# Kernel tuning notes

Hardware: AMD Instinct MI355X
Metric: run time of the kernel (lower is better)

## Reference

```python
import jax, jax.numpy as jnp
import numpy as np

B, T, C, D = 4, 20, 128, 64
TD = T * D  # 1280; adaptor input dim = 2*TD = 2560


def setup_inputs() -> dict:
    key = jax.random.key(0)
    ks = jax.random.split(key, 12)

    def lin(k, out_d, in_d):
        return jax.random.normal(k, (out_d, in_d), jnp.float32) / np.float32(np.sqrt(in_d))

    return {
        "h": jax.random.normal(ks[0], (B, T, C, D), jnp.float32),
        "W1": lin(ks[1], 128, 2 * TD), "b1": jnp.zeros((128,), jnp.float32),
        "W2": lin(ks[2], 256, 128),   "b2": jnp.zeros((256,), jnp.float32),
        "W3": lin(ks[3], 64, 256),    "b3": jnp.zeros((64,), jnp.float32),
        "W4": lin(ks[4], 1, 64),      "b4": jnp.zeros((1,), jnp.float32),
        "A_a": jax.random.normal(ks[5], (C, C), jnp.float32) * 0.01,
        "A_m": jax.random.normal(ks[6], (C, C), jnp.float32) * 0.01,
        "W_add": lin(ks[7], D, D), "b_add": jnp.zeros((D,), jnp.float32),
        "W_mod": lin(ks[8], D, D), "b_mod": jnp.zeros((D,), jnp.float32),
        "beta1": jnp.float32(1.0), "beta2": jnp.float32(1.0), "beta3": jnp.float32(1.0),
    }


def reference(h, W1, b1, W2, b2, W3, b3, W4, b4, A_a, A_m,
              W_add, b_add, W_mod, b_mod, beta1, beta2, beta3):
    Bb, Tt, Cc, Dd = h.shape
    td = Tt * Dd
    # H^(u) flattened over time: (B, C, T*D)
    h_flat = jnp.transpose(h, (0, 2, 1, 3)).reshape(Bb, Cc, td)

    # Adaptor MLP on concat(H^u, H^v). First layer is linear on the concat,
    # so split W1 and broadcast-add instead of materializing (B,C,C,2*T*D).
    W1u, W1v = W1[:, :td], W1[:, td:]
    fu = h_flat @ W1u.T                      # (B, C, 128) contribution of u
    fv = h_flat @ W1v.T                      # (B, C, 128) contribution of v
    x = jax.nn.relu(fu[:, :, None, :] + fv[:, None, :, :] + b1)   # (B, Cu, Cv, 128)
    x = jax.nn.relu(jnp.einsum('buvk,mk->buvm', x, W2) + b2)       # (B, Cu, Cv, 256)
    x = jax.nn.relu(jnp.einsum('buvk,mk->buvm', x, W3) + b3)       # (B, Cu, Cv, 64)
    s = jax.nn.sigmoid(jnp.einsum('buvk,mk->buvm', x, W4) + b4)[..., 0]  # (B, C, C)

    # Add path: a_t^(v) = sum_u S^(u,v) * A_a^(u,v) * h_t^(u)
    w = s * A_a[None]                        # (B, Cu, Cv)
    a = jnp.einsum('buv,btud->btvd', w, h)   # (B, T, C, D)
    a = a @ W_add.T + b_add

    # Modulator path: m_t^(v) = (sum_u A_m^(u,v) h_t^(u)) * h_t^(v)
    m = jnp.einsum('uv,btud->btvd', A_m, h) * h
    m = m @ W_mod.T + b_mod

    return beta1 * h + beta2 * a + beta3 * m
```

## Files before the change

### kernel.cpp

```cpp
#include <hip/hip_runtime.h>
#include <cmath>

#define NB 4
#define NT 20
#define NC 128
#define ND 64
#define TD 1280

typedef short short8 __attribute__((ext_vector_type(8)));
typedef float f32x4 __attribute__((ext_vector_type(4)));

static __device__ __forceinline__ unsigned short f2bf(float f) {
  union { float f; unsigned int u; } v; v.f = f;
  unsigned int r = v.u + 0x7FFFu + ((v.u >> 16) & 1u);
  return (unsigned short)(r >> 16);
}

static __device__ __forceinline__ void conv16(const float* __restrict__ s,
                                              unsigned short* __restrict__ d) {
#pragma unroll
  for (int q = 0; q < 2; q++) {
    float4 f0 = *(const float4*)(s + q * 8);
    float4 f1 = *(const float4*)(s + q * 8 + 4);
    uint4 o;
    o.x = (unsigned)f2bf(f0.x) | ((unsigned)f2bf(f0.y) << 16);
    o.y = (unsigned)f2bf(f0.z) | ((unsigned)f2bf(f0.w) << 16);
    o.z = (unsigned)f2bf(f1.x) | ((unsigned)f2bf(f1.y) << 16);
    o.w = (unsigned)f2bf(f1.z) | ((unsigned)f2bf(f1.w) << 16);
    *(uint4*)(d + q * 8) = o;
  }
}

static __device__ __forceinline__ void conv16_lds(const float* __restrict__ s,
                                                  char* __restrict__ base,
                                                  int byte0, int swz) {
#pragma unroll
  for (int q = 0; q < 2; q++) {
    float4 f0 = *(const float4*)(s + q * 8);
    float4 f1 = *(const float4*)(s + q * 8 + 4);
    uint4 o;
    o.x = (unsigned)f2bf(f0.x) | ((unsigned)f2bf(f0.y) << 16);
    o.y = (unsigned)f2bf(f0.z) | ((unsigned)f2bf(f0.w) << 16);
    o.z = (unsigned)f2bf(f1.x) | ((unsigned)f2bf(f1.y) << 16);
    o.w = (unsigned)f2bf(f1.z) | ((unsigned)f2bf(f1.w) << 16);
    *(uint4*)(base + ((byte0 + q * 16) ^ swz)) = o;
  }
}

__global__ __launch_bounds__(128) void k_front2(
    const float* __restrict__ h, const float* __restrict__ W1,
    const float* __restrict__ W2, const float* __restrict__ W3,
    const float* __restrict__ A_m, const float* __restrict__ W_add,
    const float* __restrict__ W_mod,
    float* __restrict__ fuv,
    unsigned short* __restrict__ W2bf, unsigned short* __restrict__ W3bf,
    unsigned short* __restrict__ A_mTbf, unsigned short* __restrict__ W_addbf,
    unsigned short* __restrict__ W_modbf, unsigned short* __restrict__ hbfT) {
  __shared__ char smem[33280];
  int blk = blockIdx.x, tid = threadIdx.x;
  if (blk < 256) {
    char* atile = smem;
    char* btile = smem + 8192;
    int mtile = blk & 15;
    int ntile = blk >> 4;
    int lane = tid & 63;
    int w = tid >> 6;
    int lr = lane & 15, lhi = lane >> 4;
    int ac = tid >> 2;
    int akseg = (tid & 3) << 5;
    int arow_g = mtile * 32 + ac;
    int ab = arow_g >> 7, acc_c = arow_g & 127;
    int aswz = (ac & 7) << 4;
    int abase = ac * 256 + akseg * 2;
    int bn = tid >> 3;
    int bkseg = (tid & 7) << 4;
    int bn_g = ntile * 16 + bn;
    const float* bsrc_row =
        W1 + (size_t)(bn_g & 127) * (2 * TD) + (bn_g >> 7) * TD;
    int bswz = (bn & 7) << 4;
    int bbase = bn * 256 + bkseg * 2;
    int arow_l = w * 16 + lr;
    int a_rd_base = arow_l * 256;
    int a_rd_swz = (lr & 7) << 4;
    int b_rd_base = lr * 256;

    f32x4 acc = (f32x4){0.f, 0.f, 0.f, 0.f};
    for (int kc = 0; kc < 10; kc++) {
      int k0 = kc * 128;
      if (kc) __syncthreads();
      {
        int t5 = (k0 + akseg) >> 6;
        int d0 = akseg & 63;
        const float* src =
            h + (((size_t)(ab * NT + t5)) * NC + acc_c) * ND + d0;
        conv16_lds(src, atile, abase, aswz);
        conv16_lds(src + 16, atile, abase + 32, aswz);
      }
      conv16_lds(bsrc_row + k0 + bkseg, btile, bbase, bswz);
      __syncthreads();
#pragma unroll
      for (int ks = 0; ks < 4; ks++) {
        int koff = ks * 64 + lhi * 16;
        short8 a = *(const short8*)(atile + a_rd_base + (koff ^ a_rd_swz));
        short8 bv = *(const short8*)(btile + b_rd_base + (koff ^ ((lr & 7) << 4)));
        acc = __builtin_amdgcn_mfma_f32_16x16x32_bf16(a, bv, acc, 0, 0, 0);
      }
    }
    int m0 = mtile * 32 + w * 16 + lhi * 4;
    int n = ntile * 16 + lr;
#pragma unroll
    for (int r = 0; r < 4; r++)
      fuv[(size_t)(m0 + r) * 256 + n] = acc[r];
    return;
  }
  int cb = blk - 256;
  if (cb < 16) {
    size_t i = (size_t)cb * 2048 + tid * 16;
    conv16(W2 + i, W2bf + i);
  } else if (cb < 24) {
    size_t i = (size_t)(cb - 16) * 2048 + tid * 16;
    conv16(W3 + i, W3bf + i);
  } else if (cb < 32) {
    size_t base = (size_t)(cb - 24) * 2048 + tid * 16;
    unsigned short tmp[16];
#pragma unroll
    for (int i2 = 0; i2 < 16; i2++) {
      size_t idx = base + i2;
      int v = (int)(idx >> 7), u = (int)(idx & 127);
      tmp[i2] = f2bf(A_m[(size_t)u * 128 + v]);
    }
    *(uint4*)(A_mTbf + base) = *(uint4*)tmp;
    *(uint4*)(A_mTbf + base + 8) = *(uint4*)(tmp + 8);
  } else if (cb < 34) {
    size_t i = (size_t)(cb - 32) * 2048 + tid * 16;
    conv16(W_add + i, W_addbf + i);
  } else if (cb < 36) {
    size_t i = (size_t)(cb - 34) * 2048 + tid * 16;
    conv16(W_mod + i, W_modbf + i);
  } else {
    float (*hsl)[65] = (float (*)[65])smem;
    int bt = cb - 36;
    const float* hb = h + (size_t)bt * 8192;
    for (int i = tid; i < 8192; i += 128) hsl[i >> 6][i & 63] = hb[i];
    __syncthreads();
    unsigned short* ob = hbfT + (size_t)bt * 8192;
    for (int i = tid; i < 8192; i += 128) {
      int d = i >> 7, u = i & 127;
      ob[i] = f2bf(hsl[u][d]);
    }
  }
}

__global__ __launch_bounds__(512) void k_pair(
    const float* __restrict__ fuv, const float* __restrict__ b1,
    const unsigned short* __restrict__ W2bf, const float* __restrict__ b2,
    const unsigned short* __restrict__ W3bf, const float* __restrict__ b3,
    const float* __restrict__ W4, const float* __restrict__ b4,
    const float* __restrict__ A_a, unsigned short* __restrict__ wTbf) {
  int blk = blockIdx.x;
  int b = blk >> 6;
  int u0 = (blk & 63) << 1;
  __shared__ char ycraw[8][4096];
  __shared__ char w2all[65536];
  __shared__ char w3all[32768];
  int t = threadIdx.x;
  int lane = t & 63;
  int w = t >> 6;
  int uw = u0 + (w >> 2);
  int lr = lane & 15;
  int lhi = lane >> 4;
  int v0w = (w & 3) * 32;
  int sw = (lr & 7) << 4;

  for (int s = w; s < 64; s += 8) {
    int o = s * 1024 + lane * 16;
    int row = o >> 8;
    int cbo = o & 255;
    const char* src = (const char*)W2bf + (size_t)row * 256 +
                      (cbo ^ ((row & 7) << 4));
    __builtin_amdgcn_global_load_lds(src, w2all + s * 1024, 16, 0, 0);
  }
  for (int s = w; s < 32; s += 8) {
    int o = s * 1024 + lane * 16;
    int row = o >> 9;
    int cbo = o & 511;
    const char* src = (const char*)W3bf + (size_t)row * 512 +
                      (cbo ^ ((row & 7) << 4));
    __builtin_amdgcn_global_load_lds(src, w3all + s * 1024, 16, 0, 0);
  }

  short8 xf[4][2];
  {
    const float* fu_base = fuv + ((size_t)(b * NC + uw)) * 256;
#pragma unroll
    for (int ks = 0; ks < 4; ks++) {
      int k0 = ks * 32 + lhi * 8;
      float4 fua = *(const float4*)(fu_base + k0);
      float4 fub4 = *(const float4*)(fu_base + k0 + 4);
      float4 b1a = *(const float4*)(b1 + k0);
      float4 b1b = *(const float4*)(b1 + k0 + 4);
#pragma unroll
      for (int vg = 0; vg < 2; vg++) {
        int v = v0w + vg * 16 + lr;
        const float* fvr = fuv + ((size_t)(b * NC + v)) * 256 + 128 + k0;
        float4 fva = *(const float4*)(fvr);
        float4 fvb = *(const float4*)(fvr + 4);
        float e[8];
        e[0] = fua.x + fva.x + b1a.x; e[1] = fua.y + fva.y + b1a.y;
        e[2] = fua.z + fva.z + b1a.z; e[3] = fua.w + fva.w + b1a.w;
        e[4] = fub4.x + fvb.x + b1b.x; e[5] = fub4.y + fvb.y + b1b.y;
        e[6] = fub4.z + fvb.z + b1b.z; e[7] = fub4.w + fvb.w + b1b.w;
        union { unsigned int pw[4]; short8 s8; } pk;
#pragma unroll
        for (int i2 = 0; i2 < 4; i2++) {
          float lo = e[2 * i2] > 0.f ? e[2 * i2] : 0.f;
          float hi = e[2 * i2 + 1] > 0.f ? e[2 * i2 + 1] : 0.f;
          pk.pw[i2] = (unsigned int)f2bf(lo) | ((unsigned int)f2bf(hi) << 16);
        }
        xf[ks][vg] = pk.s8;
      }
    }
  }
  __syncthreads();

  char* ycb = ycraw[w];
  f32x4 zacc[2][4];
#pragma unroll
  for (int q = 0; q < 2; q++)
#pragma unroll
    for (int n = 0; n < 4; n++) zacc[q][n] = (f32x4){0.f, 0.f, 0.f, 0.f};

  for (int c = 0; c < 4; c++) {
    int mc = c * 64;
    const char* w2base_c = w2all + mc * 256;
    f32x4 yac[4][2];
#pragma unroll
    for (int mt = 0; mt < 4; mt++) {
      yac[mt][0] = (f32x4){0.f, 0.f, 0.f, 0.f};
      yac[mt][1] = (f32x4){0.f, 0.f, 0.f, 0.f};
    }
    __builtin_amdgcn_s_setprio(1);
#pragma unroll
    for (int ks = 0; ks < 4; ks++) {
#pragma unroll
      for (int mt = 0; mt < 4; mt++) {
        int wrow = mt * 16 + lr;
        short8 wv = *(const short8*)(
            w2base_c + wrow * 256 + ((ks * 64 + lhi * 16) ^ ((wrow & 7) << 4)));
        yac[mt][0] = __builtin_amdgcn_mfma_f32_16x16x32_bf16(wv, xf[ks][0], yac[mt][0], 0, 0, 0);
        yac[mt][1] = __builtin_amdgcn_mfma_f32_16x16x32_bf16(wv, xf[ks][1], yac[mt][1], 0, 0, 0);
      }
    }
    __builtin_amdgcn_s_setprio(0);
#pragma unroll
    for (int mt = 0; mt < 4; mt++) {
      float4 b2v = *(const float4*)(b2 + mc + mt * 16 + lhi * 4);
#pragma unroll
      for (int vg = 0; vg < 2; vg++) {
        int v = vg * 16 + lr;
        float e0 = yac[mt][vg][0] + b2v.x; e0 = e0 > 0.f ? e0 : 0.f;
        float e1 = yac[mt][vg][1] + b2v.y; e1 = e1 > 0.f ? e1 : 0.f;
        float e2 = yac[mt][vg][2] + b2v.z; e2 = e2 > 0.f ? e2 : 0.f;
        float e3 = yac[mt][vg][3] + b2v.w; e3 = e3 > 0.f ? e3 : 0.f;
        uint2 pw;
        pw.x = (unsigned)f2bf(e0) | ((unsigned)f2bf(e1) << 16);
        pw.y = (unsigned)f2bf(e2) | ((unsigned)f2bf(e3) << 16);
        int byte = (v * 128 + (mt * 16 + lhi * 4) * 2) ^ ((lr & 7) << 4);
        *(uint2*)(ycb + byte) = pw;
      }
    }
    __builtin_amdgcn_s_setprio(1);
#pragma unroll
    for (int ks2 = 0; ks2 < 2; ks2++) {
      int kb = ks2 * 32 + lhi * 8;
      short8 ya0 = *(const short8*)(ycb + ((lr * 128 + kb * 2) ^ sw));
      short8 ya1 = *(const short8*)(ycb + (((16 + lr) * 128 + kb * 2) ^ sw));
#pragma unroll
      for (int n = 0; n < 4; n++) {
        int jrow = 16 * n + lr;
        short8 w3v = *(const short8*)(
            w3all + jrow * 512 +
            ((mc * 2 + ks2 * 64 + lhi * 16) ^ ((jrow & 7) << 4)));
        zacc[0][n] = __builtin_amdgcn_mfma_f32_16x16x32_bf16(ya0, w3v, zacc[0][n], 0, 0, 0);
        zacc[1][n] = __builtin_amdgcn_mfma_f32_16x16x32_bf16(ya1, w3v, zacc[1][n], 0, 0, 0);
      }
    }
    __builtin_amdgcn_s_setprio(0);
  }

  float sp[2][4];
#pragma unroll
  for (int q = 0; q < 2; q++)
#pragma unroll
    for (int r = 0; r < 4; r++) sp[q][r] = 0.f;
#pragma unroll
  for (int n = 0; n < 4; n++) {
    int j = 16 * n + lr;
    float b3v = b3[j], w4v = W4[j];
#pragma unroll
    for (int q = 0; q < 2; q++)
#pragma unroll
      for (int r = 0; r < 4; r++) {
        float z = zacc[q][n][r] + b3v;
        z = z > 0.f ? z : 0.f;
        sp[q][r] += w4v * z;
      }
  }
#pragma unroll
  for (int mask = 1; mask <= 8; mask <<= 1)
#pragma unroll
    for (int q = 0; q < 2; q++)
#pragma unroll
      for (int r = 0; r < 4; r++)
        sp[q][r] += __shfl_xor(sp[q][r], mask, 64);
  float bb4 = b4[0];
  if (lr == 0) {
#pragma unroll
    for (int q = 0; q < 2; q++)
#pragma unroll
      for (int r = 0; r < 4; r++) {
        int v = v0w + 16 * q + lhi * 4 + r;
        float s = 1.f / (1.f + expf(-(sp[q][r] + bb4)));
        wTbf[((size_t)(b * NC + v)) * NC + uw] = f2bf(s * A_a[uw * NC + v]);
      }
  }
}

__global__ __launch_bounds__(128) void k_out_mfma(
    const float* __restrict__ h, const unsigned short* __restrict__ wTbf,
    const unsigned short* __restrict__ A_mTbf,
    const unsigned short* __restrict__ hbfT,
    const unsigned short* __restrict__ W_addbf,
    const unsigned short* __restrict__ W_modbf,
    const float* __restrict__ b_add, const float* __restrict__ b_mod,
    const float* __restrict__ beta1p, const float* __restrict__ beta2p,
    const float* __restrict__ beta3p, float* __restrict__ out) {
  int blk = blockIdx.x;
  int bt = blk >> 3;
  int v0 = (blk & 7) << 4;
  int b = bt / 20;
  __shared__ char apre_l[2048];
  __shared__ char mpre_l[2048];
  int t = threadIdx.x;
  int lane = t & 63;
  int w = t >> 6;
  int lr = lane & 15, lhi = lane >> 4;
  int nf0 = w * 2;

  f32x4 aacc[2], macc[2];
#pragma unroll
  for (int i = 0; i < 2; i++) {
    aacc[i] = (f32x4){0.f, 0.f, 0.f, 0.f};
    macc[i] = (f32x4){0.f, 0.f, 0.f, 0.f};
  }
  const unsigned short* wrow = wTbf + ((size_t)(b * NC + v0 + lr)) * NC + lhi * 8;
  const unsigned short* arow = A_mTbf + (size_t)(v0 + lr) * NC + lhi * 8;
  const unsigned short* hTrow = hbfT + (size_t)bt * 8192 + lhi * 8;
#pragma unroll
  for (int kb = 0; kb < 128; kb += 32) {
    short8 aw = *(const short8*)(wrow + kb);
    short8 am = *(const short8*)(arow + kb);
#pragma unroll
    for (int nfi = 0; nfi < 2; nfi++) {
      int nf = nf0 + nfi;
      short8 bv = *(const short8*)(hTrow + (size_t)(nf * 16 + lr) * NC + kb);
      aacc[nfi] = __builtin_amdgcn_mfma_f32_16x16x32_bf16(aw, bv, aacc[nfi], 0, 0, 0);
      macc[nfi] = __builtin_amdgcn_mfma_f32_16x16x32_bf16(am, bv, macc[nfi], 0, 0, 0);
    }
  }

  float hval[2][4];
  const float* hbase = h + (size_t)bt * 8192;
#pragma unroll
  for (int nfi = 0; nfi < 2; nfi++) {
    int d = (nf0 + nfi) * 16 + lr;
#pragma unroll
    for (int r = 0; r < 4; r++) {
      int vl = lhi * 4 + r;
      float hv = hbase[(size_t)(v0 + vl) * 64 + d];
      hval[nfi][r] = hv;
      int byte = (vl * 128 + d * 2) ^ ((vl & 7) << 4);
      *(unsigned short*)(apre_l + byte) = f2bf(aacc[nfi][r]);
      *(unsigned short*)(mpre_l + byte) = f2bf(macc[nfi][r] * hv);
    }
  }
  __syncthreads();

  f32x4 oa[2], om[2];
#pragma unroll
  for (int i = 0; i < 2; i++) {
    oa[i] = (f32x4){0.f, 0.f, 0.f, 0.f};
    om[i] = (f32x4){0.f, 0.f, 0.f, 0.f};
  }
  int sw = (lr & 7) << 4;
#pragma unroll
  for (int kb = 0; kb < 64; kb += 32) {
    int off0 = lr * 128 + kb * 2 + lhi * 16;
    short8 pa = *(const short8*)(apre_l + (off0 ^ sw));
    short8 pm = *(const short8*)(mpre_l + (off0 ^ sw));
#pragma unroll
    for (int nfi = 0; nfi < 2; nfi++) {
      int nf = nf0 + nfi;
      const unsigned short* wa = W_addbf + (size_t)(nf * 16 + lr) * 64 + kb + lhi * 8;
      const unsigned short* wm = W_modbf + (size_t)(nf * 16 + lr) * 64 + kb + lhi * 8;
      short8 wav = *(const short8*)wa;
      short8 wmv = *(const short8*)wm;
      oa[nfi] = __builtin_amdgcn_mfma_f32_16x16x32_bf16(pa, wav, oa[nfi], 0, 0, 0);
      om[nfi] = __builtin_amdgcn_mfma_f32_16x16x32_bf16(pm, wmv, om[nfi], 0, 0, 0);
    }
  }
  float bb1 = beta1p[0], bb2 = beta2p[0], bb3 = beta3p[0];
  float* obase = out + (size_t)bt * 8192 + (size_t)v0 * 64;
#pragma unroll
  for (int nfi = 0; nfi < 2; nfi++) {
    int d = (nf0 + nfi) * 16 + lr;
    float ba = b_add[d], bm = b_mod[d];
#pragma unroll
    for (int r = 0; r < 4; r++) {
      int vl = lhi * 4 + r;
      obase[(size_t)vl * 64 + d] =
          bb1 * hval[nfi][r] + bb2 * (oa[nfi][r] + ba) + bb3 * (om[nfi][r] + bm);
    }
  }
}

extern "C" void kernel_launch(void* const* d_in, const int* in_sizes, int n_in,
                              void* d_out, int out_size, void* d_ws, size_t ws_size,
                              hipStream_t stream) {
  const float* h     = (const float*)d_in[0];
  const float* W1    = (const float*)d_in[1];
  const float* b1    = (const float*)d_in[2];
  const float* W2    = (const float*)d_in[3];
  const float* b2    = (const float*)d_in[4];
  const float* W3    = (const float*)d_in[5];
  const float* b3    = (const float*)d_in[6];
  const float* W4    = (const float*)d_in[7];
  const float* b4    = (const float*)d_in[8];
  const float* A_a   = (const float*)d_in[9];
  const float* A_m   = (const float*)d_in[10];
  const float* W_add = (const float*)d_in[11];
  const float* b_add = (const float*)d_in[12];
  const float* W_mod = (const float*)d_in[13];
  const float* b_mod = (const float*)d_in[14];
  const float* beta1 = (const float*)d_in[15];
  const float* beta2 = (const float*)d_in[16];
  const float* beta3 = (const float*)d_in[17];
  float* out = (float*)d_out;

  char* ws = (char*)d_ws;
  float* fuv             = (float*)(ws);
  unsigned short* wTbf   = (unsigned short*)(ws + 512 * 1024);
  unsigned short* A_mTbf = (unsigned short*)(ws + 640 * 1024);
  unsigned short* W_addbf= (unsigned short*)(ws + 672 * 1024);
  unsigned short* W_modbf= (unsigned short*)(ws + 680 * 1024);
  unsigned short* W2bf   = (unsigned short*)(ws + 688 * 1024);
  unsigned short* W3bf   = (unsigned short*)(ws + 752 * 1024);
  unsigned short* hbfT   = (unsigned short*)(ws + 784 * 1024);

  k_front2<<<372, 128, 0, stream>>>(h, W1, W2, W3, A_m, W_add, W_mod,
                                    fuv, W2bf, W3bf, A_mTbf, W_addbf, W_modbf,
                                    hbfT);
  k_pair<<<256, 512, 0, stream>>>(fuv, b1, W2bf, b2, W3bf, b3, W4, b4, A_a, wTbf);
  k_out_mfma<<<640, 128, 0, stream>>>(h, wTbf, A_mTbf, hbfT, W_addbf, W_modbf,
                                      b_add, b_mod, beta1, beta2, beta3, out);
}
```

Measured before the change: 40.26 us.

## Double-buffer front GEMM tiles and keep W3 fragments in registers

```diff
diff --git a/kernel.cpp b/kernel.cpp
--- a/kernel.cpp
+++ b/kernel.cpp
@@ -59,8 +59,10 @@
   __shared__ char smem[33280];
   int blk = blockIdx.x, tid = threadIdx.x;
   if (blk < 256) {
-    char* atile = smem;
-    char* btile = smem + 8192;
+    char* atile0 = smem;
+    char* atile1 = smem + 8192;
+    char* btile0 = smem + 16384;
+    char* btile1 = smem + 20480;
     int mtile = blk & 15;
     int ntile = blk >> 4;
     int lane = tid & 63;
@@ -83,28 +85,40 @@
     int a_rd_base = arow_l * 256;
     int a_rd_swz = (lr & 7) << 4;
     int b_rd_base = lr * 256;
+    int ad0 = akseg & 63;
+
+    {
+      int t5 = akseg >> 6;
+      const float* src = h + (((size_t)(ab * NT + t5)) * NC + acc_c) * ND + ad0;
+      conv16_lds(src, atile0, abase, aswz);
+      conv16_lds(src + 16, atile0, abase + 32, aswz);
+      conv16_lds(bsrc_row + bkseg, btile0, bbase, bswz);
+    }
+    __syncthreads();
 
     f32x4 acc = (f32x4){0.f, 0.f, 0.f, 0.f};
     for (int kc = 0; kc < 10; kc++) {
-      int k0 = kc * 128;
-      if (kc) __syncthreads();
-      {
-        int t5 = (k0 + akseg) >> 6;
-        int d0 = akseg & 63;
+      if (kc < 9) {
+        int k1 = (kc + 1) * 128;
+        char* an = ((kc + 1) & 1) ? atile1 : atile0;
+        char* bnx = ((kc + 1) & 1) ? btile1 : btile0;
+        int t5 = (k1 + akseg) >> 6;
         const float* src =
-            h + (((size_t)(ab * NT + t5)) * NC + acc_c) * ND + d0;
-        conv16_lds(src, atile, abase, aswz);
-        conv16_lds(src + 16, atile, abase + 32, aswz);
-      }
-      conv16_lds(bsrc_row + k0 + bkseg, btile, bbase, bswz);
-      __syncthreads();
+            h + (((size_t)(ab * NT + t5)) * NC + acc_c) * ND + ad0;
+        conv16_lds(src, an, abase, aswz);
+        conv16_lds(src + 16, an, abase + 32, aswz);
+        conv16_lds(bsrc_row + k1 + bkseg, bnx, bbase, bswz);
+      }
+      const char* at = (kc & 1) ? atile1 : atile0;
+      const char* bt = (kc & 1) ? btile1 : btile0;
 #pragma unroll
       for (int ks = 0; ks < 4; ks++) {
         int koff = ks * 64 + lhi * 16;
-        short8 a = *(const short8*)(atile + a_rd_base + (koff ^ a_rd_swz));
-        short8 bv = *(const short8*)(btile + b_rd_base + (koff ^ ((lr & 7) << 4)));
+        short8 a = *(const short8*)(at + a_rd_base + (koff ^ a_rd_swz));
+        short8 bv = *(const short8*)(bt + b_rd_base + (koff ^ ((lr & 7) << 4)));
         acc = __builtin_amdgcn_mfma_f32_16x16x32_bf16(a, bv, acc, 0, 0, 0);
       }
+      __syncthreads();
     }
     int m0 = mtile * 32 + w * 16 + lhi * 4;
     int n = ntile * 16 + lr;
@@ -162,7 +176,6 @@
   int u0 = (blk & 63) << 1;
   __shared__ char ycraw[8][4096];
   __shared__ char w2all[65536];
-  __shared__ char w3all[32768];
   int t = threadIdx.x;
   int lane = t & 63;
   int w = t >> 6;
@@ -180,13 +193,18 @@
                       (cbo ^ ((row & 7) << 4));
     __builtin_amdgcn_global_load_lds(src, w2all + s * 1024, 16, 0, 0);
   }
-  for (int s = w; s < 32; s += 8) {
-    int o = s * 1024 + lane * 16;
-    int row = o >> 9;
-    int cbo = o & 511;
-    const char* src = (const char*)W3bf + (size_t)row * 512 +
-                      (cbo ^ ((row & 7) << 4));
-    __builtin_amdgcn_global_load_lds(src, w3all + s * 1024, 16, 0, 0);
+
+  short8 w3f[4][2][4];
+  {
+    const unsigned short* w3base = W3bf + (size_t)lr * 256 + lhi * 8;
+#pragma unroll
+    for (int c = 0; c < 4; c++)
+#pragma unroll
+      for (int ks2 = 0; ks2 < 2; ks2++)
+#pragma unroll
+        for (int n = 0; n < 4; n++)
+          w3f[c][ks2][n] = *(const short8*)(
+              w3base + (size_t)(16 * n) * 256 + c * 64 + ks2 * 32);
   }
 
   short8 xf[4][2];
@@ -230,6 +248,7 @@
 #pragma unroll
     for (int n = 0; n < 4; n++) zacc[q][n] = (f32x4){0.f, 0.f, 0.f, 0.f};
 
+#pragma unroll
   for (int c = 0; c < 4; c++) {
     int mc = c * 64;
     const char* w2base_c = w2all + mc * 256;
@@ -277,12 +296,8 @@
       short8 ya1 = *(const short8*)(ycb + (((16 + lr) * 128 + kb * 2) ^ sw));
 #pragma unroll
       for (int n = 0; n < 4; n++) {
-        int jrow = 16 * n + lr;
-        short8 w3v = *(const short8*)(
-            w3all + jrow * 512 +
-            ((mc * 2 + ks2 * 64 + lhi * 16) ^ ((jrow & 7) << 4)));
-        zacc[0][n] = __builtin_amdgcn_mfma_f32_16x16x32_bf16(ya0, w3v, zacc[0][n], 0, 0, 0);
-        zacc[1][n] = __builtin_amdgcn_mfma_f32_16x16x32_bf16(ya1, w3v, zacc[1][n], 0, 0, 0);
+        zacc[0][n] = __builtin_amdgcn_mfma_f32_16x16x32_bf16(ya0, w3f[c][ks2][n], zacc[0][n], 0, 0, 0);
+        zacc[1][n] = __builtin_amdgcn_mfma_f32_16x16x32_bf16(ya1, w3f[c][ks2][n], zacc[1][n], 0, 0, 0);
       }
     }
     __builtin_amdgcn_s_setprio(0);
```

After: 46.45 us. 15.4% more time.
